# Performance work log

Measured on AMD Instinct MI355X. Metric: run time of the kernel, lower is better.

## Reference

```python
import jax, jax.numpy as jnp
import numpy as np

B, LQ, LK, D, H = 16, 1024, 1024, 512, 8
DK = D // H  # 64
EPS = 1e-5


def _ln(x, g, b):
    m = jnp.mean(x, axis=-1, keepdims=True)
    v = jnp.mean((x - m) ** 2, axis=-1, keepdims=True)
    return (x - m) * jax.lax.rsqrt(v + EPS) * g + b


def _rotate_every_two(x):
    # x: (..., d) with d even; pairs (x1,x2) -> (-x2, x1) interleaved
    x1 = x[..., 0::2]
    x2 = x[..., 1::2]
    return jnp.stack((-x2, x1), axis=-1).reshape(x.shape)


def setup_inputs() -> dict:
    key = jax.random.key(0)
    ks = jax.random.split(key, 16)
    s = 1.0 / np.sqrt(D)
    inp = {
        "satellite": jax.random.normal(ks[0], (B, LK, D), jnp.float32),
        "satellite_pos_embedding": jax.random.normal(ks[1], (2, B, LK, D), jnp.float32),
        "timeseries": jax.random.normal(ks[2], (B, LQ, D), jnp.float32),
        "timeseries_pos_embedding": jax.random.normal(ks[3], (2, B, LQ, D), jnp.float32),
        "ln_sat_g": jnp.ones((D,), jnp.float32),
        "ln_sat_b": jnp.zeros((D,), jnp.float32),
        "ln_ts_g": jnp.ones((D,), jnp.float32),
        "ln_ts_b": jnp.zeros((D,), jnp.float32),
        "Wv": jax.random.normal(ks[4], (D, DK), jnp.float32) * s,
        "bv": jnp.zeros((DK,), jnp.float32),
        "Wq": jax.random.normal(ks[5], (H, D, DK), jnp.float32) * s,
        "bq": jnp.zeros((H, DK), jnp.float32),
        "Wk": jax.random.normal(ks[6], (H, D, DK), jnp.float32) * s,
        "bk": jnp.zeros((H, DK), jnp.float32),
        "Wsat": jax.random.normal(ks[7], (H, D, DK), jnp.float32) * s,
        "bsat": jnp.zeros((H, DK), jnp.float32),
        "Wts": jax.random.normal(ks[8], (H, D, DK), jnp.float32) * s,
        "bts": jnp.zeros((H, DK), jnp.float32),
        "Wh": jax.random.normal(ks[9], (DK, D), jnp.float32) * (1.0 / np.sqrt(DK)),
    }
    return inp


def reference(satellite, satellite_pos_embedding, timeseries, timeseries_pos_embedding,
              ln_sat_g, ln_sat_b, ln_ts_g, ln_ts_b,
              Wv, bv, Wq, bq, Wk, bk, Wsat, bsat, Wts, bts, Wh):
    sat = _ln(satellite, ln_sat_g, ln_sat_b)      # (B,LK,D)
    ts = _ln(timeseries, ln_ts_g, ln_ts_b)        # (B,LQ,D)

    v = ts @ jnp.zeros_like(Wv) if False else sat @ Wv + bv  # (B,LK,DK), shared across heads

    # batched per-head projections
    q = jnp.einsum('bld,hdk->bhlk', ts, Wq) + bq[:, None, :]    # (B,H,LQ,DK)
    k = jnp.einsum('bld,hdk->bhlk', sat, Wk) + bk[:, None, :]   # (B,H,LK,DK)

    sin_sat = jnp.einsum('bld,hdk->bhlk', satellite_pos_embedding[0], Wsat) + bsat[:, None, :]
    cos_sat = jnp.einsum('bld,hdk->bhlk', satellite_pos_embedding[1], Wsat) + bsat[:, None, :]
    sin_ts = jnp.einsum('bld,hdk->bhlk', timeseries_pos_embedding[0], Wts) + bts[:, None, :]
    cos_ts = jnp.einsum('bld,hdk->bhlk', timeseries_pos_embedding[1], Wts) + bts[:, None, :]

    # rotary (dim_rotary == DK, so no pass-through part)
    q = q * cos_ts + _rotate_every_two(q) * sin_ts
    k = k * cos_sat + _rotate_every_two(k) * sin_sat

    scale = jnp.sqrt(jnp.asarray(DK, q.dtype))
    scores = jnp.einsum('bhqd,bhkd->bhqk', q, k) / scale        # (B,H,LQ,LK)
    attn = jax.nn.softmax(scores, axis=-1)
    head = jnp.einsum('bhqk,bkd->bhqd', attn, v)                # (B,H,LQ,DK)

    out = jnp.mean(head, axis=1) @ Wh                           # (B,LQ,D)
    attn_out = jnp.transpose(attn, (0, 2, 1, 3))                # (B,LQ,H,LK) matches torch.stack(dim=2)
    return (out, attn_out)
```

## Files before the change

kernel.cpp:

```cpp
#include <hip/hip_runtime.h>

#define OUT_OFF 8388608ull

typedef __attribute__((ext_vector_type(4))) float f32x4;
typedef __attribute__((ext_vector_type(8))) __bf16 bf16x8;
typedef __attribute__((ext_vector_type(8))) unsigned short us8;

__device__ __forceinline__ unsigned short f2b(float f) {
  return __builtin_bit_cast(unsigned short, (__bf16)f);
}
__device__ __forceinline__ float b2f(unsigned short u) {
  return (float)__builtin_bit_cast(__bf16, u);
}
__device__ __forceinline__ bf16x8 ldfrag(const unsigned short* p) {
  return __builtin_bit_cast(bf16x8, *(const us8*)p);
}
__device__ __forceinline__ bf16x8 ldsfrag(const unsigned short* base, int byte_off) {
  return __builtin_bit_cast(bf16x8, *(const us8*)((const char*)base + byte_off));
}
__device__ __forceinline__ f32x4 mfma16(bf16x8 a, bf16x8 b, f32x4 c) {
  return __builtin_amdgcn_mfma_f32_16x16x32_bf16(a, b, c, 0, 0, 0);
}
__device__ __forceinline__ void stage8_f32(unsigned short* dst, const float* src) {
  const f32x4 x = *(const f32x4*)src;
  const f32x4 y = *(const f32x4*)(src + 4);
  us8 v;
  v[0]=f2b(x[0]); v[1]=f2b(x[1]); v[2]=f2b(x[2]); v[3]=f2b(x[3]);
  v[4]=f2b(y[0]); v[5]=f2b(y[1]); v[6]=f2b(y[2]); v[7]=f2b(y[3]);
  *(us8*)dst = v;
}
__device__ __forceinline__ void stage8_split(unsigned short* dh, unsigned short* dl, const float* src) {
  const f32x4 x = *(const f32x4*)src;
  const f32x4 y = *(const f32x4*)(src + 4);
  us8 h, l;
  #pragma unroll
  for (int i = 0; i < 4; ++i) {
    unsigned short hv = f2b(x[i]); h[i] = hv; l[i] = f2b(x[i] - b2f(hv));
  }
  #pragma unroll
  for (int i = 0; i < 4; ++i) {
    unsigned short hv = f2b(y[i]); h[4+i] = hv; l[4+i] = f2b(y[i] - b2f(hv));
  }
  *(us8*)dh = h; *(us8*)dl = l;
}
__device__ __forceinline__ void stage8_bf(unsigned short* dst, const unsigned short* src) {
  *(us8*)dst = *(const us8*)src;
}

__global__ __launch_bounds__(256) void repack_kernel(
    const float* __restrict__ Wq, const float* __restrict__ Wk,
    const float* __restrict__ Wsat, const float* __restrict__ Wts,
    const float* __restrict__ Wv, const float* __restrict__ Wh,
    unsigned short* __restrict__ Wq_h, unsigned short* __restrict__ Wq_l,
    unsigned short* __restrict__ Wk_h, unsigned short* __restrict__ Wk_l,
    unsigned short* __restrict__ Wsat_h, unsigned short* __restrict__ Wsat_l,
    unsigned short* __restrict__ Wts_h, unsigned short* __restrict__ Wts_l,
    float* __restrict__ Wv_t, float* __restrict__ Wh_t)
{
  int i = blockIdx.x * 256 + threadIdx.x;
  if (i < 1048576) {
    int seg = i >> 18, j = i & 262143;
    int n = j >> 9, d = j & 511;
    const float* W = (seg == 0) ? Wq : (seg == 1) ? Wk : (seg == 2) ? Wsat : Wts;
    unsigned short* Oh = (seg == 0) ? Wq_h : (seg == 1) ? Wk_h : (seg == 2) ? Wsat_h : Wts_h;
    unsigned short* Ol = (seg == 0) ? Wq_l : (seg == 1) ? Wk_l : (seg == 2) ? Wsat_l : Wts_l;
    float w = W[((n >> 6) * 512 + d) * 64 + (n & 63)];
    unsigned short h = f2b(w);
    Oh[j] = h; Ol[j] = f2b(w - b2f(h));
  } else if (i < 1081344) {
    int j = i - 1048576; int dk = j >> 9, d = j & 511;
    Wv_t[j] = Wv[d * 64 + dk];
  } else if (i < 1114112) {
    int j = i - 1081344; int d = j >> 6, dk = j & 63;
    Wh_t[j] = Wh[dk * 512 + d];
  }
}

__global__ __launch_bounds__(256) void ln_kernel(
    const float* __restrict__ sat, const float* __restrict__ ts,
    const float* __restrict__ gs, const float* __restrict__ bs,
    const float* __restrict__ gt, const float* __restrict__ bt,
    unsigned short* __restrict__ sat_h, unsigned short* __restrict__ sat_l,
    unsigned short* __restrict__ ts_h, unsigned short* __restrict__ ts_l)
{
  int row = blockIdx.x;
  const float* x; unsigned short *yh, *yl; const float* g; const float* bb;
  if (row < 16384) {
    x = sat + (size_t)row * 512; yh = sat_h + (size_t)row * 512; yl = sat_l + (size_t)row * 512;
    g = gs; bb = bs;
  } else {
    int r = row - 16384;
    x = ts + (size_t)r * 512; yh = ts_h + (size_t)r * 512; yl = ts_l + (size_t)r * 512;
    g = gt; bb = bt;
  }
  int t = threadIdx.x;
  float x0 = x[t], x1 = x[t + 256];
  float s = x0 + x1, s2 = x0 * x0 + x1 * x1;
  #pragma unroll
  for (int o = 1; o < 64; o <<= 1) { s += __shfl_xor(s, o); s2 += __shfl_xor(s2, o); }
  __shared__ float red[8];
  int w = t >> 6;
  if ((t & 63) == 0) { red[w] = s; red[4 + w] = s2; }
  __syncthreads();
  float S  = red[0] + red[1] + red[2] + red[3];
  float S2 = red[4] + red[5] + red[6] + red[7];
  float mean = S * (1.f / 512.f);
  float inv = rsqrtf(S2 * (1.f / 512.f) - mean * mean + 1e-5f);
  float y0 = (x0 - mean) * inv * g[t]       + bb[t];
  float y1 = (x1 - mean) * inv * g[t + 256] + bb[t + 256];
  unsigned short h0 = f2b(y0), h1 = f2b(y1);
  yh[t] = h0;       yl[t] = f2b(y0 - b2f(h0));
  yh[t + 256] = h1; yl[t + 256] = f2b(y1 - b2f(h1));
}

__global__ __launch_bounds__(256) void proj_rope_kernel(
    const unsigned short* __restrict__ Axm_h, const unsigned short* __restrict__ Axm_l,
    const float* __restrict__ Axs, const float* __restrict__ Axc,
    const unsigned short* __restrict__ Bm_h, const unsigned short* __restrict__ Bm_l,
    const unsigned short* __restrict__ Br_h, const unsigned short* __restrict__ Br_l,
    const float* __restrict__ bm_, const float* __restrict__ br_,
    unsigned short* __restrict__ out_h, unsigned short* __restrict__ out_l)
{
  __shared__ __attribute__((aligned(16))) unsigned short
      sAmH[64*40], sAmL[64*40], sAsH[64*40], sAsL[64*40], sAcH[64*40], sAcL[64*40],
      sBmH[64*40], sBmL[64*40], sBrH[64*40], sBrL[64*40];
  const int tid = threadIdx.x;
  const int lane = tid & 63, wid = tid >> 6;
  const int wy = wid >> 1, wx = wid & 1;
  const int m0 = blockIdx.x * 64, n0 = blockIdx.y * 64;
  const int srow = tid >> 2, sc8 = (tid & 3) * 8;
  const int sidx = srow * 40 + sc8;

  f32x4 accM[2][2] = {}, accS[2][2] = {}, accC[2][2] = {};

  for (int k0 = 0; k0 < 512; k0 += 32) {
    const size_t ao = (size_t)(m0 + srow) * 512 + k0 + sc8;
    stage8_bf(&sAmH[sidx], Axm_h + ao);
    stage8_bf(&sAmL[sidx], Axm_l + ao);
    stage8_split(&sAsH[sidx], &sAsL[sidx], Axs + ao);
    stage8_split(&sAcH[sidx], &sAcL[sidx], Axc + ao);
    const size_t bo = (size_t)(n0 + srow) * 512 + k0 + sc8;
    stage8_bf(&sBmH[sidx], Bm_h + bo);
    stage8_bf(&sBmL[sidx], Bm_l + bo);
    stage8_bf(&sBrH[sidx], Br_h + bo);
    stage8_bf(&sBrL[sidx], Br_l + bo);
    __syncthreads();
    const int q8 = (lane >> 4) * 8;
    const int fm = (wy * 32 + (lane & 15)) * 40 + q8;
    const int fn = (wx * 32 + (lane & 15)) * 40 + q8;
    bf16x8 amh0 = ldfrag(&sAmH[fm]), amh1 = ldfrag(&sAmH[fm + 640]);
    bf16x8 aml0 = ldfrag(&sAmL[fm]), aml1 = ldfrag(&sAmL[fm + 640]);
    bf16x8 ash0 = ldfrag(&sAsH[fm]), ash1 = ldfrag(&sAsH[fm + 640]);
    bf16x8 asl0 = ldfrag(&sAsL[fm]), asl1 = ldfrag(&sAsL[fm + 640]);
    bf16x8 ach0 = ldfrag(&sAcH[fm]), ach1 = ldfrag(&sAcH[fm + 640]);
    bf16x8 acl0 = ldfrag(&sAcL[fm]), acl1 = ldfrag(&sAcL[fm + 640]);
    bf16x8 bmh0 = ldfrag(&sBmH[fn]), bmh1 = ldfrag(&sBmH[fn + 640]);
    bf16x8 bml0 = ldfrag(&sBmL[fn]), bml1 = ldfrag(&sBmL[fn + 640]);
    bf16x8 brh0 = ldfrag(&sBrH[fn]), brh1 = ldfrag(&sBrH[fn + 640]);
    bf16x8 brl0 = ldfrag(&sBrL[fn]), brl1 = ldfrag(&sBrL[fn + 640]);
    accM[0][0] = mfma16(amh0, bmh0, accM[0][0]); accM[0][1] = mfma16(amh0, bmh1, accM[0][1]);
    accM[1][0] = mfma16(amh1, bmh0, accM[1][0]); accM[1][1] = mfma16(amh1, bmh1, accM[1][1]);
    accM[0][0] = mfma16(amh0, bml0, accM[0][0]); accM[0][1] = mfma16(amh0, bml1, accM[0][1]);
    accM[1][0] = mfma16(amh1, bml0, accM[1][0]); accM[1][1] = mfma16(amh1, bml1, accM[1][1]);
    accM[0][0] = mfma16(aml0, bmh0, accM[0][0]); accM[0][1] = mfma16(aml0, bmh1, accM[0][1]);
    accM[1][0] = mfma16(aml1, bmh0, accM[1][0]); accM[1][1] = mfma16(aml1, bmh1, accM[1][1]);
    accS[0][0] = mfma16(ash0, brh0, accS[0][0]); accS[0][1] = mfma16(ash0, brh1, accS[0][1]);
    accS[1][0] = mfma16(ash1, brh0, accS[1][0]); accS[1][1] = mfma16(ash1, brh1, accS[1][1]);
    accS[0][0] = mfma16(ash0, brl0, accS[0][0]); accS[0][1] = mfma16(ash0, brl1, accS[0][1]);
    accS[1][0] = mfma16(ash1, brl0, accS[1][0]); accS[1][1] = mfma16(ash1, brl1, accS[1][1]);
    accS[0][0] = mfma16(asl0, brh0, accS[0][0]); accS[0][1] = mfma16(asl0, brh1, accS[0][1]);
    accS[1][0] = mfma16(asl1, brh0, accS[1][0]); accS[1][1] = mfma16(asl1, brh1, accS[1][1]);
    accC[0][0] = mfma16(ach0, brh0, accC[0][0]); accC[0][1] = mfma16(ach0, brh1, accC[0][1]);
    accC[1][0] = mfma16(ach1, brh0, accC[1][0]); accC[1][1] = mfma16(ach1, brh1, accC[1][1]);
    accC[0][0] = mfma16(ach0, brl0, accC[0][0]); accC[0][1] = mfma16(ach0, brl1, accC[0][1]);
    accC[1][0] = mfma16(ach1, brl0, accC[1][0]); accC[1][1] = mfma16(ach1, brl1, accC[1][1]);
    accC[0][0] = mfma16(acl0, brh0, accC[0][0]); accC[0][1] = mfma16(acl0, brh1, accC[0][1]);
    accC[1][0] = mfma16(acl1, brh0, accC[1][0]); accC[1][1] = mfma16(acl1, brh1, accC[1][1]);
    __syncthreads();
  }

  const int col = lane & 15, quad = lane >> 4;
  #pragma unroll
  for (int nt = 0; nt < 2; ++nt) {
    const int n = n0 + wx * 32 + nt * 16 + col;
    const float bmv = bm_[n], brv = br_[n];
    const int h = n >> 6, dk = n & 63;
    const float sgn = (n & 1) ? 1.f : -1.f;
    #pragma unroll
    for (int mt = 0; mt < 2; ++mt) {
      #pragma unroll
      for (int r = 0; r < 4; ++r) {
        float qv = accM[mt][nt][r] + bmv;
        float sv = accS[mt][nt][r] + brv;
        float cv = accC[mt][nt][r] + brv;
        float qo = __shfl_xor(qv, 1);
        float res = qv * cv + sgn * qo * sv;
        const int m = m0 + wy * 32 + mt * 16 + quad * 4 + r;
        const int b = m >> 10, l = m & 1023;
        const size_t idx = (((size_t)(b * 8 + h) * 1024 + l) << 6) + dk;
        unsigned short hv = f2b(res);
        out_h[idx] = hv;
        out_l[idx] = f2b(res - b2f(hv));
      }
    }
  }
}

__global__ __launch_bounds__(256) void fused_attn_kernel(
    const unsigned short* __restrict__ q_h, const unsigned short* __restrict__ q_l,
    const unsigned short* __restrict__ k_h, const unsigned short* __restrict__ k_l,
    const unsigned short* __restrict__ vt,
    float* __restrict__ attn, float* __restrict__ out_pre)
{
  __shared__ __attribute__((aligned(16))) unsigned short sK[8192];
  __shared__ __attribute__((aligned(16))) unsigned short sP[16384];
  __shared__ float redM[16][4];
  __shared__ float redS[16][4];

  const int tid  = threadIdx.x;
  const int lane = tid & 63, wid = tid >> 6;
  const int col  = lane & 15, quad = lane >> 4;
  const int q0   = blockIdx.x * 16;
  const int z    = blockIdx.y;
  const int b    = z >> 3;
  const size_t zoff = (size_t)z << 16;

  const size_t qoff = zoff + (size_t)(q0 + col) * 64 + quad * 8;
  const bf16x8 aQh0 = ldfrag(q_h + qoff), aQh1 = ldfrag(q_h + qoff + 32);
  const bf16x8 aQl0 = ldfrag(q_l + qoff), aQl1 = ldfrag(q_l + qoff + 32);

  us8 kreg[4];
  const unsigned short* ksrc[4];
  int kdst[4];
  #pragma unroll
  for (int i = 0; i < 4; ++i) {
    const int s = tid + i * 256;
    const int plane = s >> 9, r = (s >> 3) & 63, c = s & 7;
    ksrc[i] = (plane ? k_l : k_h) + zoff + (size_t)r * 64 + c * 8;
    kdst[i] = plane * 8192 + r * 128 + ((c ^ (r & 7)) << 4);
  }
  #pragma unroll
  for (int i = 0; i < 4; ++i) kreg[i] = *(const us8*)(ksrc[i]);

  const int nl  = wid * 16 + col;
  const int sx  = nl & 7;
  const int bh0_off = nl * 128 + ((quad ^ sx) << 4);
  const int bh1_off = nl * 128 + (((4 + quad) ^ sx) << 4);
  const int bl0_off = 8192 + bh0_off;
  const int bl1_off = 8192 + bh1_off;

  f32x4 acc[16];
  #pragma unroll
  for (int kt = 0; kt < 16; ++kt) acc[kt] = (f32x4){0.f, 0.f, 0.f, 0.f};

  #pragma unroll
  for (int kt = 0; kt < 16; ++kt) {
    __syncthreads();
    #pragma unroll
    for (int i = 0; i < 4; ++i) *(us8*)((char*)sK + kdst[i]) = kreg[i];
    __syncthreads();
    if (kt < 15) {
      #pragma unroll
      for (int i = 0; i < 4; ++i) kreg[i] = *(const us8*)(ksrc[i] + (kt + 1) * 4096);
    }
    bf16x8 bh0 = ldsfrag(sK, bh0_off), bh1 = ldsfrag(sK, bh1_off);
    bf16x8 bl0 = ldsfrag(sK, bl0_off), bl1 = ldsfrag(sK, bl1_off);
    acc[kt] = mfma16(aQh0, bh0, acc[kt]);
    acc[kt] = mfma16(aQh0, bl0, acc[kt]);
    acc[kt] = mfma16(aQl0, bh0, acc[kt]);
    acc[kt] = mfma16(aQh1, bh1, acc[kt]);
    acc[kt] = mfma16(aQh1, bl1, acc[kt]);
    acc[kt] = mfma16(aQl1, bh1, acc[kt]);
  }

  float pm[4];
  #pragma unroll
  for (int r = 0; r < 4; ++r) pm[r] = acc[0][r];
  #pragma unroll
  for (int kt = 1; kt < 16; ++kt)
    #pragma unroll
    for (int r = 0; r < 4; ++r) pm[r] = fmaxf(pm[r], acc[kt][r]);
  #pragma unroll
  for (int o = 1; o < 16; o <<= 1)
    #pragma unroll
    for (int r = 0; r < 4; ++r) pm[r] = fmaxf(pm[r], __shfl_xor(pm[r], o));
  if (col == 0)
    #pragma unroll
    for (int r = 0; r < 4; ++r) redM[quad * 4 + r][wid] = pm[r];
  __syncthreads();
  float M_[4];
  #pragma unroll
  for (int r = 0; r < 4; ++r) {
    const float* q = redM[quad * 4 + r];
    M_[r] = fmaxf(fmaxf(q[0], q[1]), fmaxf(q[2], q[3]));
  }
  float ps[4] = {0.f, 0.f, 0.f, 0.f};
  #pragma unroll
  for (int kt = 0; kt < 16; ++kt)
    #pragma unroll
    for (int r = 0; r < 4; ++r) {
      float p = __expf((acc[kt][r] - M_[r]) * 0.125f);
      acc[kt][r] = p; ps[r] += p;
    }
  #pragma unroll
  for (int o = 1; o < 16; o <<= 1)
    #pragma unroll
    for (int r = 0; r < 4; ++r) ps[r] += __shfl_xor(ps[r], o);
  if (col == 0)
    #pragma unroll
    for (int r = 0; r < 4; ++r) redS[quad * 4 + r][wid] = ps[r];
  __syncthreads();
  float rinv[4];
  #pragma unroll
  for (int r = 0; r < 4; ++r) {
    const float* q = redS[quad * 4 + r];
    rinv[r] = 1.f / (q[0] + q[1] + q[2] + q[3]);
  }

  const size_t arow = ((((size_t)b << 10) + q0) * 8 + (z & 7)) << 10;
  #pragma unroll
  for (int kt = 0; kt < 16; ++kt) {
    const int cg = kt * 64 + wid * 16 + col;
    #pragma unroll
    for (int r = 0; r < 4; ++r) {
      const int row = quad * 4 + r;
      const float pn = acc[kt][r] * rinv[r];
      attn[arow + (size_t)row * 8192 + cg] = pn;
      *(unsigned short*)((char*)sP + ((row * 2048 + cg * 2) ^ ((row & 7) << 4))) = f2b(pn);
    }
  }
  __syncthreads();

  f32x4 o4 = (f32x4){0.f, 0.f, 0.f, 0.f};
  const unsigned short* vb = vt + ((size_t)b << 16) + (size_t)(wid * 16 + col) * 1024;
  const int prow = col * 2048;
  const int pswz = (col & 7) << 4;
  #pragma unroll 4
  for (int k0 = 0; k0 < 1024; k0 += 32) {
    bf16x8 a  = ldsfrag(sP, prow + (((k0 + quad * 8) * 2) ^ pswz));
    bf16x8 bv = ldfrag(vb + k0 + quad * 8);
    o4 = mfma16(a, bv, o4);
  }
  const size_t obase = ((size_t)b << 16) + (size_t)(q0 + quad * 4) * 64 + wid * 16 + col;
  #pragma unroll
  for (int r = 0; r < 4; ++r) atomicAdd(&out_pre[obase + (size_t)r * 64], o4[r]);
}

enum { MODE_V = 0, MODE_OUT = 3 };

template<int MODE>
__global__ __launch_bounds__(256) void mfma_gemm(
    const void* __restrict__ Ap, const void* __restrict__ Bp,
    const float* __restrict__ bias, void* __restrict__ Outp)
{
  constexpr bool A_BF  = (MODE == MODE_V);
  constexpr int  LDA   = (MODE == MODE_V) ? 512 : 64;
  constexpr int  LDB   = (MODE == MODE_V) ? 512 : 64;
  constexpr int  KTOT  = (MODE == MODE_V) ? 512 : 64;
  constexpr float SCALE = (MODE == MODE_V) ? 0.125f : 1.0f;

  __shared__ __attribute__((aligned(16))) unsigned short sA[64*40], sB[64*40];
  const int tid = threadIdx.x;
  const int lane = tid & 63, wid = tid >> 6;
  const int wy = wid >> 1, wx = wid & 1;
  const int m0 = blockIdx.x * 64, n0 = blockIdx.y * 64;
  const int srow = tid >> 2, sc8 = (tid & 3) * 8;
  const int sidx = srow * 40 + sc8;

  const float* Af = (const float*)Ap;  const unsigned short* Ab = (const unsigned short*)Ap;
  const float* Bf = (const float*)Bp;

  f32x4 acc[2][2] = {};

  for (int k0 = 0; k0 < KTOT; k0 += 32) {
    { const size_t ao = (size_t)(m0 + srow) * LDA + k0 + sc8;
      if constexpr (A_BF) stage8_bf(&sA[sidx], Ab + ao); else stage8_f32(&sA[sidx], Af + ao); }
    { const size_t bo = (size_t)(n0 + srow) * LDB + k0 + sc8;
      stage8_f32(&sB[sidx], Bf + bo); }
    __syncthreads();
    const int q8 = (lane >> 4) * 8;
    const int fm = (wy * 32 + (lane & 15)) * 40 + q8;
    const int fn = (wx * 32 + (lane & 15)) * 40 + q8;
    bf16x8 a0 = ldfrag(&sA[fm]), a1 = ldfrag(&sA[fm + 640]);
    bf16x8 b0 = ldfrag(&sB[fn]), b1 = ldfrag(&sB[fn + 640]);
    acc[0][0] = mfma16(a0, b0, acc[0][0]); acc[0][1] = mfma16(a0, b1, acc[0][1]);
    acc[1][0] = mfma16(a1, b0, acc[1][0]); acc[1][1] = mfma16(a1, b1, acc[1][1]);
    __syncthreads();
  }

  const int col = lane & 15, quad = lane >> 4;
  #pragma unroll
  for (int nt = 0; nt < 2; ++nt) {
    const int n = n0 + wx * 32 + nt * 16 + col;
    const float bv = bias ? bias[n] : 0.f;
    #pragma unroll
    for (int mt = 0; mt < 2; ++mt) {
      #pragma unroll
      for (int r = 0; r < 4; ++r) {
        const int m = m0 + wy * 32 + mt * 16 + quad * 4 + r;
        const float v = (acc[mt][nt][r] + bv) * SCALE;
        if constexpr (MODE == MODE_V) {
          ((unsigned short*)Outp)[((size_t)(m >> 10) << 16) + ((size_t)n << 10) + (m & 1023)] = f2b(v);
        } else {
          ((float*)Outp)[(size_t)m * 512 + n] = v;
        }
      }
    }
  }
}

extern "C" void kernel_launch(void* const* d_in, const int* in_sizes, int n_in,
                              void* d_out, int out_size, void* d_ws, size_t ws_size,
                              hipStream_t stream)
{
  const float* satellite  = (const float*)d_in[0];
  const float* sat_pos    = (const float*)d_in[1];
  const float* timeseries = (const float*)d_in[2];
  const float* ts_pos     = (const float*)d_in[3];
  const float* ln_sat_g   = (const float*)d_in[4];
  const float* ln_sat_b   = (const float*)d_in[5];
  const float* ln_ts_g    = (const float*)d_in[6];
  const float* ln_ts_b    = (const float*)d_in[7];
  const float* Wv  = (const float*)d_in[8];
  const float* bv  = (const float*)d_in[9];
  const float* Wq  = (const float*)d_in[10];
  const float* bq  = (const float*)d_in[11];
  const float* Wk  = (const float*)d_in[12];
  const float* bk  = (const float*)d_in[13];
  const float* Wsat= (const float*)d_in[14];
  const float* bsat= (const float*)d_in[15];
  const float* Wts = (const float*)d_in[16];
  const float* bts = (const float*)d_in[17];
  const float* Wh  = (const float*)d_in[18];

  char* ws = (char*)d_ws;
  unsigned short* sat_h = (unsigned short*)(ws + 0);
  unsigned short* sat_l = (unsigned short*)(ws + 16777216);
  unsigned short* ts_h  = (unsigned short*)(ws + 33554432);
  unsigned short* ts_l  = (unsigned short*)(ws + 50331648);
  unsigned short* q_hi  = (unsigned short*)(ws + 67108864);
  unsigned short* k_hi  = (unsigned short*)(ws + 83886080);
  unsigned short* vt    = (unsigned short*)(ws + 100663296);
  float* out_pre        = (float*)(ws + 102760448);
  char* wb = ws + 106954752;
  unsigned short* Wq_h   = (unsigned short*)(wb + 0);
  unsigned short* Wq_l   = (unsigned short*)(wb + 524288);
  unsigned short* Wk_h   = (unsigned short*)(wb + 1048576);
  unsigned short* Wk_l   = (unsigned short*)(wb + 1572864);
  unsigned short* Wsat_h = (unsigned short*)(wb + 2097152);
  unsigned short* Wsat_l = (unsigned short*)(wb + 2621440);
  unsigned short* Wts_h  = (unsigned short*)(wb + 3145728);
  unsigned short* Wts_l  = (unsigned short*)(wb + 3670016);
  float* Wv_t            = (float*)(wb + 4194304);
  float* Wh_t            = (float*)(wb + 4325376);

  float* outF = (float*)d_out;
  float* attn = outF + OUT_OFF;
  unsigned short* q_lo = (unsigned short*)d_out;
  unsigned short* k_lo = (unsigned short*)d_out + 8388608;

  repack_kernel<<<4352, 256, 0, stream>>>(Wq, Wk, Wsat, Wts, Wv, Wh,
      Wq_h, Wq_l, Wk_h, Wk_l, Wsat_h, Wsat_l, Wts_h, Wts_l, Wv_t, Wh_t);
  ln_kernel<<<32768, 256, 0, stream>>>(satellite, timeseries, ln_sat_g, ln_sat_b,
                                       ln_ts_g, ln_ts_b, sat_h, sat_l, ts_h, ts_l);
  proj_rope_kernel<<<dim3(256, 8), 256, 0, stream>>>(
      ts_h, ts_l, ts_pos, ts_pos + 8388608, Wq_h, Wq_l, Wts_h, Wts_l, bq, bts, q_hi, q_lo);
  proj_rope_kernel<<<dim3(256, 8), 256, 0, stream>>>(
      sat_h, sat_l, sat_pos, sat_pos + 8388608, Wk_h, Wk_l, Wsat_h, Wsat_l, bk, bsat, k_hi, k_lo);
  mfma_gemm<MODE_V><<<dim3(256, 1, 1), 256, 0, stream>>>(sat_h, Wv_t, bv, vt);
  hipMemsetAsync(out_pre, 0, 16384 * 64 * 4, stream);
  fused_attn_kernel<<<dim3(64, 128), 256, 0, stream>>>(
      q_hi, q_lo, k_hi, k_lo, vt, attn, out_pre);
  mfma_gemm<MODE_OUT><<<dim3(256, 8, 1), 256, 0, stream>>>(out_pre, Wh_t, nullptr, outF);
}
```

Measured before the change: 1.280 ms.

## Write per-head attention outputs directly and fold head mean into output GEMM

The attention kernel now writes each head's P·V result to its own slot in an (B*LQ, 8*64) buffer with plain stores. This replaces the atomicAdd accumulation and the memset. The head mean is folded into the output GEMM by replicating Wh eight times along K, and the GEMM's A operand is split into hi and lo bf16 planes for accuracy. The P staging buffer now reuses the K shared memory in four chunks, which lowers LDS use and may raise occupancy. The K prefetch is moved ahead of the second barrier. The trade-off is an output GEMM with 8x larger K plus extra MFMAs for the lo plane, and more barriers in the P·V phase.

```diff
diff --git a/kernel.cpp b/kernel.cpp
--- a/kernel.cpp
+++ b/kernel.cpp
@@ -55,7 +55,7 @@
     unsigned short* __restrict__ Wk_h, unsigned short* __restrict__ Wk_l,
     unsigned short* __restrict__ Wsat_h, unsigned short* __restrict__ Wsat_l,
     unsigned short* __restrict__ Wts_h, unsigned short* __restrict__ Wts_l,
-    float* __restrict__ Wv_t, float* __restrict__ Wh_t)
+    float* __restrict__ Wv_t, float* __restrict__ Wh_t8)
 {
   int i = blockIdx.x * 256 + threadIdx.x;
   if (i < 1048576) {
@@ -70,9 +70,9 @@
   } else if (i < 1081344) {
     int j = i - 1048576; int dk = j >> 9, d = j & 511;
     Wv_t[j] = Wv[d * 64 + dk];
-  } else if (i < 1114112) {
-    int j = i - 1081344; int d = j >> 6, dk = j & 63;
-    Wh_t[j] = Wh[dk * 512 + d];
+  } else if (i < 1343488) {
+    int j = i - 1081344; int d = j >> 9, n = j & 511;
+    Wh_t8[j] = Wh[(n & 63) * 512 + d];
   }
 }
 
@@ -210,19 +210,19 @@
     const unsigned short* __restrict__ q_h, const unsigned short* __restrict__ q_l,
     const unsigned short* __restrict__ k_h, const unsigned short* __restrict__ k_l,
     const unsigned short* __restrict__ vt,
-    float* __restrict__ attn, float* __restrict__ out_pre)
+    float* __restrict__ attn, float* __restrict__ out_pre8)
 {
   __shared__ __attribute__((aligned(16))) unsigned short sK[8192];
-  __shared__ __attribute__((aligned(16))) unsigned short sP[16384];
   __shared__ float redM[16][4];
   __shared__ float redS[16][4];
+  unsigned short* sP = sK;
 
   const int tid  = threadIdx.x;
   const int lane = tid & 63, wid = tid >> 6;
   const int col  = lane & 15, quad = lane >> 4;
   const int q0   = blockIdx.x * 16;
   const int z    = blockIdx.y;
-  const int b    = z >> 3;
+  const int b    = z >> 3, h = z & 7;
   const size_t zoff = (size_t)z << 16;
 
   const size_t qoff = zoff + (size_t)(q0 + col) * 64 + quad * 8;
@@ -258,11 +258,12 @@
     __syncthreads();
     #pragma unroll
     for (int i = 0; i < 4; ++i) *(us8*)((char*)sK + kdst[i]) = kreg[i];
-    __syncthreads();
     if (kt < 15) {
       #pragma unroll
-      for (int i = 0; i < 4; ++i) kreg[i] = *(const us8*)(ksrc[i] + (kt + 1) * 4096);
-    }
+      for (int i = 0; i < 4; ++i)
+        kreg[i] = *(const us8*)(ksrc[i] + (kt + 1) * 4096);
+    }
+    __syncthreads();
     bf16x8 bh0 = ldsfrag(sK, bh0_off), bh1 = ldsfrag(sK, bh1_off);
     bf16x8 bl0 = ldsfrag(sK, bl0_off), bl1 = ldsfrag(sK, bl1_off);
     acc[kt] = mfma16(aQh0, bh0, acc[kt]);
@@ -317,33 +318,39 @@
     rinv[r] = 1.f / (q[0] + q[1] + q[2] + q[3]);
   }
 
-  const size_t arow = ((((size_t)b << 10) + q0) * 8 + (z & 7)) << 10;
-  #pragma unroll
-  for (int kt = 0; kt < 16; ++kt) {
-    const int cg = kt * 64 + wid * 16 + col;
-    #pragma unroll
-    for (int r = 0; r < 4; ++r) {
-      const int row = quad * 4 + r;
-      const float pn = acc[kt][r] * rinv[r];
-      attn[arow + (size_t)row * 8192 + cg] = pn;
-      *(unsigned short*)((char*)sP + ((row * 2048 + cg * 2) ^ ((row & 7) << 4))) = f2b(pn);
-    }
-  }
-  __syncthreads();
-
+  const size_t arow = ((((size_t)b << 10) + q0) * 8 + h) << 10;
   f32x4 o4 = (f32x4){0.f, 0.f, 0.f, 0.f};
   const unsigned short* vb = vt + ((size_t)b << 16) + (size_t)(wid * 16 + col) * 1024;
-  const int prow = col * 2048;
+  const int prow = col * 512;
   const int pswz = (col & 7) << 4;
-  #pragma unroll 4
-  for (int k0 = 0; k0 < 1024; k0 += 32) {
-    bf16x8 a  = ldsfrag(sP, prow + (((k0 + quad * 8) * 2) ^ pswz));
-    bf16x8 bv = ldfrag(vb + k0 + quad * 8);
-    o4 = mfma16(a, bv, o4);
-  }
-  const size_t obase = ((size_t)b << 16) + (size_t)(q0 + quad * 4) * 64 + wid * 16 + col;
-  #pragma unroll
-  for (int r = 0; r < 4; ++r) atomicAdd(&out_pre[obase + (size_t)r * 64], o4[r]);
+  #pragma unroll
+  for (int c = 0; c < 4; ++c) {
+    __syncthreads();
+    #pragma unroll
+    for (int kk = 0; kk < 4; ++kk) {
+      const int kt = c * 4 + kk;
+      const int cg = kt * 64 + wid * 16 + col;
+      const int cl = kk * 64 + wid * 16 + col;
+      #pragma unroll
+      for (int r = 0; r < 4; ++r) {
+        const int row = quad * 4 + r;
+        const float pn = acc[kt][r] * rinv[r];
+        attn[arow + (size_t)row * 8192 + cg] = pn;
+        *(unsigned short*)((char*)sP + ((row * 512 + cl * 2) ^ ((row & 7) << 4))) = f2b(pn);
+      }
+    }
+    __syncthreads();
+    #pragma unroll
+    for (int k0 = 0; k0 < 256; k0 += 32) {
+      bf16x8 a  = ldsfrag(sP, prow + (((k0 + quad * 8) * 2) ^ pswz));
+      bf16x8 bv = ldfrag(vb + c * 256 + k0 + quad * 8);
+      o4 = mfma16(a, bv, o4);
+    }
+  }
+
+  const size_t obase = (((size_t)b << 10) + q0 + quad * 4) * 512 + h * 64 + wid * 16 + col;
+  #pragma unroll
+  for (int r = 0; r < 4; ++r) out_pre8[obase + (size_t)r * 512] = o4[r];
 }
 
 enum { MODE_V = 0, MODE_OUT = 3 };
@@ -354,12 +361,10 @@
     const float* __restrict__ bias, void* __restrict__ Outp)
 {
   constexpr bool A_BF  = (MODE == MODE_V);
-  constexpr int  LDA   = (MODE == MODE_V) ? 512 : 64;
-  constexpr int  LDB   = (MODE == MODE_V) ? 512 : 64;
-  constexpr int  KTOT  = (MODE == MODE_V) ? 512 : 64;
   constexpr float SCALE = (MODE == MODE_V) ? 0.125f : 1.0f;
 
   __shared__ __attribute__((aligned(16))) unsigned short sA[64*40], sB[64*40];
+  __shared__ __attribute__((aligned(16))) unsigned short sAl[A_BF ? 16 : 64*40];
   const int tid = threadIdx.x;
   const int lane = tid & 63, wid = tid >> 6;
   const int wy = wid >> 1, wx = wid & 1;
@@ -372,10 +377,11 @@
 
   f32x4 acc[2][2] = {};
 
-  for (int k0 = 0; k0 < KTOT; k0 += 32) {
-    { const size_t ao = (size_t)(m0 + srow) * LDA + k0 + sc8;
-      if constexpr (A_BF) stage8_bf(&sA[sidx], Ab + ao); else stage8_f32(&sA[sidx], Af + ao); }
-    { const size_t bo = (size_t)(n0 + srow) * LDB + k0 + sc8;
+  for (int k0 = 0; k0 < 512; k0 += 32) {
+    { const size_t ao = (size_t)(m0 + srow) * 512 + k0 + sc8;
+      if constexpr (A_BF) stage8_bf(&sA[sidx], Ab + ao);
+      else                stage8_split(&sA[sidx], &sAl[sidx], Af + ao); }
+    { const size_t bo = (size_t)(n0 + srow) * 512 + k0 + sc8;
       stage8_f32(&sB[sidx], Bf + bo); }
     __syncthreads();
     const int q8 = (lane >> 4) * 8;
@@ -385,6 +391,11 @@
     bf16x8 b0 = ldfrag(&sB[fn]), b1 = ldfrag(&sB[fn + 640]);
     acc[0][0] = mfma16(a0, b0, acc[0][0]); acc[0][1] = mfma16(a0, b1, acc[0][1]);
     acc[1][0] = mfma16(a1, b0, acc[1][0]); acc[1][1] = mfma16(a1, b1, acc[1][1]);
+    if constexpr (!A_BF) {
+      bf16x8 al0 = ldfrag(&sAl[fm]), al1 = ldfrag(&sAl[fm + 640]);
+      acc[0][0] = mfma16(al0, b0, acc[0][0]); acc[0][1] = mfma16(al0, b1, acc[0][1]);
+      acc[1][0] = mfma16(al1, b0, acc[1][0]); acc[1][1] = mfma16(al1, b1, acc[1][1]);
+    }
     __syncthreads();
   }
 
@@ -441,7 +452,8 @@
   unsigned short* q_hi  = (unsigned short*)(ws + 67108864);
   unsigned short* k_hi  = (unsigned short*)(ws + 83886080);
   unsigned short* vt    = (unsigned short*)(ws + 100663296);
-  float* out_pre        = (float*)(ws + 102760448);
+  float* Wh_t8          = (float*)(ws + 102760448);
+  float* out_pre8       = (float*)(ws + 0);
   char* wb = ws + 106954752;
   unsigned short* Wq_h   = (unsigned short*)(wb + 0);
   unsigned short* Wq_l   = (unsigned short*)(wb + 524288);
@@ -452,15 +464,14 @@
   unsigned short* Wts_h  = (unsigned short*)(wb + 3145728);
   unsigned short* Wts_l  = (unsigned short*)(wb + 3670016);
   float* Wv_t            = (float*)(wb + 4194304);
-  float* Wh_t            = (float*)(wb + 4325376);
 
   float* outF = (float*)d_out;
   float* attn = outF + OUT_OFF;
   unsigned short* q_lo = (unsigned short*)d_out;
   unsigned short* k_lo = (unsigned short*)d_out + 8388608;
 
-  repack_kernel<<<4352, 256, 0, stream>>>(Wq, Wk, Wsat, Wts, Wv, Wh,
-      Wq_h, Wq_l, Wk_h, Wk_l, Wsat_h, Wsat_l, Wts_h, Wts_l, Wv_t, Wh_t);
+  repack_kernel<<<5248, 256, 0, stream>>>(Wq, Wk, Wsat, Wts, Wv, Wh,
+      Wq_h, Wq_l, Wk_h, Wk_l, Wsat_h, Wsat_l, Wts_h, Wts_l, Wv_t, Wh_t8);
   ln_kernel<<<32768, 256, 0, stream>>>(satellite, timeseries, ln_sat_g, ln_sat_b,
                                        ln_ts_g, ln_ts_b, sat_h, sat_l, ts_h, ts_l);
   proj_rope_kernel<<<dim3(256, 8), 256, 0, stream>>>(
@@ -468,8 +479,7 @@
   proj_rope_kernel<<<dim3(256, 8), 256, 0, stream>>>(
       sat_h, sat_l, sat_pos, sat_pos + 8388608, Wk_h, Wk_l, Wsat_h, Wsat_l, bk, bsat, k_hi, k_lo);
   mfma_gemm<MODE_V><<<dim3(256, 1, 1), 256, 0, stream>>>(sat_h, Wv_t, bv, vt);
-  hipMemsetAsync(out_pre, 0, 16384 * 64 * 4, stream);
   fused_attn_kernel<<<dim3(64, 128), 256, 0, stream>>>(
-      q_hi, q_lo, k_hi, k_lo, vt, attn, out_pre);
-  mfma_gemm<MODE_OUT><<<dim3(256, 8, 1), 256, 0, stream>>>(out_pre, Wh_t, nullptr, outF);
-}
+      q_hi, q_lo, k_hi, k_lo, vt, attn, out_pre8);
+  mfma_gemm<MODE_OUT><<<dim3(256, 8, 1), 256, 0, stream>>>(out_pre8, Wh_t8, nullptr, outF);
+}
```

Result: no change. 1.304 ms (+1.9%).
